# Performance work log

Hardware: AMD Instinct MI355X
Metric: run time of the kernel (lower is better)

The kernel has to match this reference:

```python
import jax, jax.numpy as jnp
import numpy as np

B, D, K = 8192, 512, 4096
MAX_WORD_LENGTH = 16
RESIDUAL_THRESHOLD = 0.01
DECAY_FACTOR = 0.95
EPS_TARGET = 1e-8


def setup_inputs() -> dict:
    key = jax.random.key(0)
    k1, k2 = jax.random.split(key)
    targets = jax.random.normal(k1, (B, D), dtype=jnp.float32)
    codebook = jax.random.normal(k2, (K, D), dtype=jnp.float32)
    return {"targets": targets, "codebook": codebook}


def reference(targets, codebook):
    """Batched greedy residual pursuit (allow_negative_signs=True).

    Returns:
      seq      [B, L] int32 signed indices (>=0: add idx; <0: subtract (-idx-1)); 0 where inactive
      mask     [B, L] bool, True where a step actually emitted a symbol
      residual [B, D] final residual after pursuit
    """
    target_norm = jnp.linalg.norm(targets, axis=-1)  # [B]

    def step(residual, step_idx):
        rnorm = jnp.linalg.norm(residual, axis=-1)  # [B]
        active = (rnorm >= RESIDUAL_THRESHOLD) & (target_norm >= EPS_TARGET)
        # cosine similarity of each codebook vector with residual direction
        res_dir = residual / jnp.maximum(rnorm, 1e-12)[:, None]
        cos = jnp.einsum('bd,kd->bk', res_dir, codebook)  # [B, K]
        best = jnp.argmax(jnp.abs(cos), axis=-1)  # [B]
        best_cos = jnp.take_along_axis(cos, best[:, None], axis=-1)[:, 0]
        signed = jnp.where(best_cos >= 0, best, -(best + 1)).astype(jnp.int32)
        sign = jnp.where(best_cos >= 0, 1.0, -1.0).astype(residual.dtype)
        decay = jnp.power(jnp.asarray(DECAY_FACTOR, residual.dtype),
                          (step_idx + 1).astype(residual.dtype))
        contrib = sign[:, None] * decay * codebook[best]  # [B, D]
        new_res = jnp.where(active[:, None], residual - contrib, residual)
        out_idx = jnp.where(active, signed, 0)
        return new_res, (out_idx, active)

    residual, (seq, mask) = jax.lax.scan(step, targets, jnp.arange(MAX_WORD_LENGTH))
    return seq.T, mask.T, residual
```

## Files before the change

kernel.cpp:

```cpp
#include <hip/hip_runtime.h>
#include <hip/hip_bf16.h>

#define B_SZ 8192
#define D_SZ 512
#define K_SZ 4096
#define L_SZ 16
#define M_ALL (B_SZ + K_SZ)

typedef __attribute__((ext_vector_type(8))) short short8v;
typedef __attribute__((ext_vector_type(4))) float f32x4;
typedef _Float16 half8v __attribute__((ext_vector_type(8)));
typedef _Float16 h2 __attribute__((ext_vector_type(2)));
struct H2x4 { h2 a, b, c, d; };

static __device__ __forceinline__ h2 habs2(h2 a) {
    unsigned u = __builtin_bit_cast(unsigned, a) & 0x7FFF7FFFu;
    return __builtin_bit_cast(h2, u);
}
static __device__ __forceinline__ h2 hmax2(h2 a, h2 b) {
#if __has_builtin(__builtin_elementwise_max)
    return __builtin_elementwise_max(a, b);
#else
    h2 r; r[0] = a[0] > b[0] ? a[0] : b[0]; r[1] = a[1] > b[1] ? a[1] : b[1]; return r;
#endif
}

__global__ void cast_bf16_kernel(const float* __restrict__ targets,
                                 const float* __restrict__ codebook,
                                 __hip_bfloat16* __restrict__ abf) {
    int idx = blockIdx.x * blockDim.x + threadIdx.x;
    const int total4 = (M_ALL * D_SZ) / 4;
    if (idx >= total4) return;
    int base = idx * 4;
    const float* src = (base < B_SZ * D_SZ) ? (targets + base)
                                            : (codebook + (base - B_SZ * D_SZ));
    float4 v = *(const float4*)src;
    abf[base + 0] = __float2bfloat16(v.x);
    abf[base + 1] = __float2bfloat16(v.y);
    abf[base + 2] = __float2bfloat16(v.z);
    abf[base + 3] = __float2bfloat16(v.w);
}

__global__ void cn2_kernel(const float* __restrict__ codebook,
                           double* __restrict__ cn2) {
    int row  = blockIdx.x * 4 + (threadIdx.x >> 6);
    int lane = threadIdx.x & 63;
    const float* r = codebook + (size_t)row * D_SZ;
    double s = 0.0;
#pragma unroll
    for (int j = 0; j < 8; j++) { double v = (double)r[lane + 64 * j]; s += v * v; }
#pragma unroll
    for (int o = 32; o > 0; o >>= 1) s += __shfl_down(s, o, 64);
    if (lane == 0) cn2[row] = s;
}

#define BM 128
#define BN 128
#define BK 32
#define LDSS 40

__global__ __launch_bounds__(256, 2)
void gemm_bt_kernel(const __hip_bfloat16* __restrict__ A,
                    const __hip_bfloat16* __restrict__ Bm,
                    _Float16* __restrict__ C) {
    __shared__ short As[BM * LDSS];
    __shared__ short Bs[BN * LDSS];
    const int tid  = threadIdx.x;
    const int bm   = blockIdx.y * BM;
    const int bn   = blockIdx.x * BN;
    const int wave = tid >> 6, lane = tid & 63;
    const int wm = (wave & 1) * 64, wn = (wave >> 1) * 64;
    const int row16 = lane & 15, quad = lane >> 4;
    const int koff = quad * 8;

    f32x4 acc[4][4] = {};

    const int srow = tid >> 1;
    const int scol = (tid & 1) * 16;
    const short* Ag = (const short*)A;
    const short* Bg = (const short*)Bm;

    for (int k0 = 0; k0 < D_SZ; k0 += BK) {
        short8v a0 = *(const short8v*)(Ag + (size_t)(bm + srow) * D_SZ + k0 + scol);
        short8v a1 = *(const short8v*)(Ag + (size_t)(bm + srow) * D_SZ + k0 + scol + 8);
        short8v b0 = *(const short8v*)(Bg + (size_t)(bn + srow) * D_SZ + k0 + scol);
        short8v b1 = *(const short8v*)(Bg + (size_t)(bn + srow) * D_SZ + k0 + scol + 8);
        __syncthreads();
        *(short8v*)(As + srow * LDSS + scol)     = a0;
        *(short8v*)(As + srow * LDSS + scol + 8) = a1;
        *(short8v*)(Bs + srow * LDSS + scol)     = b0;
        *(short8v*)(Bs + srow * LDSS + scol + 8) = b1;
        __syncthreads();

        short8v af[4], bf[4];
#pragma unroll
        for (int i = 0; i < 4; i++)
            af[i] = *(const short8v*)(As + (wm + i * 16 + row16) * LDSS + koff);
#pragma unroll
        for (int j = 0; j < 4; j++)
            bf[j] = *(const short8v*)(Bs + (wn + j * 16 + row16) * LDSS + koff);
#pragma unroll
        for (int i = 0; i < 4; i++)
#pragma unroll
            for (int j = 0; j < 4; j++)
                acc[i][j] = __builtin_amdgcn_mfma_f32_16x16x32_bf16(af[i], bf[j], acc[i][j], 0, 0, 0);
    }

#pragma unroll
    for (int i = 0; i < 4; i++) {
        int grow = bm + wm + i * 16 + quad * 4;
#pragma unroll
        for (int j = 0; j < 4; j++) {
            int gcol = bn + wn + j * 16 + row16;
#pragma unroll
            for (int r = 0; r < 4; r++)
                C[(size_t)(grow + r) * K_SZ + gcol] = (_Float16)acc[i][j][r];
        }
    }
}

#define MAXC 16
#define MARGIN 1.5f

__global__ __launch_bounds__(256, 4)
void pursuit_kernel(const float* __restrict__ targets,
                    const float* __restrict__ codebook,
                    const _Float16* __restrict__ S,
                    const double* __restrict__ cn2,
                    float* __restrict__ out) {
    const int wave = threadIdx.x >> 6;
    const int lane = threadIdx.x & 63;
    const int b = blockIdx.x * 4 + wave;
    const int lane8 = lane * 8;

    __shared__ alignas(16) _Float16 g_s[4][K_SZ];
    __shared__ int s_cnt[4];
    __shared__ int s_cand[4][MAXC];
    _Float16* g = g_s[wave];
    int* cnt  = &s_cnt[wave];
    int* cand = s_cand[wave];

    h2 tmax; tmax[0] = (_Float16)0; tmax[1] = (_Float16)0;
    {
        const _Float16* g0 = S + (size_t)b * K_SZ + lane8;
#pragma unroll
        for (int c = 0; c < 8; c++) {
            half8v h = *(const half8v*)(g0 + c * 512);
            *(half8v*)&g[c * 512 + lane8] = h;
            H2x4 u = __builtin_bit_cast(H2x4, h);
            tmax = hmax2(tmax, hmax2(hmax2(habs2(u.a), habs2(u.b)),
                                     hmax2(habs2(u.c), habs2(u.d))));
        }
    }
    float m = fmaxf((float)tmax[0], (float)tmax[1]);

    double rres[8];
    double loc = 0.0;
    {
        const float* tg = targets + (size_t)b * D_SZ + lane8;
        float4 t0 = *(const float4*)tg;
        float4 t1 = *(const float4*)(tg + 4);
        rres[0] = t0.x; rres[1] = t0.y; rres[2] = t0.z; rres[3] = t0.w;
        rres[4] = t1.x; rres[5] = t1.y; rres[6] = t1.z; rres[7] = t1.w;
#pragma unroll
        for (int e = 0; e < 8; e++) loc += rres[e] * rres[e];
    }
#pragma unroll
    for (int o = 32; o > 0; o >>= 1) loc += __shfl_xor(loc, o, 64);
    double rn2 = loc;
    const bool tgt_ok = (sqrt(loc) >= 1e-8);

    float* out_seq  = out + (size_t)b * L_SZ;
    float* out_mask = out + (size_t)B_SZ * L_SZ + (size_t)b * L_SZ;
    float* out_res  = out + (size_t)2 * B_SZ * L_SZ + (size_t)b * D_SZ;

    double decay = 1.0;

    for (int t = 0; t < L_SZ; t++) {
        decay *= 0.95;
        bool active = (sqrt(rn2) >= 0.01) && tgt_ok;
        if (!active) {
            if (lane == 0)
                for (int tt = t; tt < L_SZ; tt++) { out_seq[tt] = 0.0f; out_mask[tt] = 0.0f; }
            break;
        }

        float M = m;
#pragma unroll
        for (int o = 32; o > 0; o >>= 1) M = fmaxf(M, __shfl_xor(M, o, 64));
        float thr = M - MARGIN;

        if (lane == 0) *cnt = 0;
        if (m >= thr) {
#pragma unroll
            for (int c = 0; c < 8; c++) {
                half8v h = *(const half8v*)&g[c * 512 + lane8];
#pragma unroll
                for (int e = 0; e < 8; e++) {
                    float f = fabsf((float)h[e]);
                    if (f >= thr) {
                        int q = atomicAdd(cnt, 1);
                        if (q < MAXC) cand[q] = c * 512 + lane8 + e;
                    }
                }
            }
        }
        __threadfence_block();
        int nc = min(*cnt, MAXC);

        int bk; double bv;
        float4 c0, c1;
        if (nc == 1) {
            bk = __builtin_amdgcn_readfirstlane(cand[0]);
            const float* cr = codebook + (size_t)bk * D_SZ + lane8;
            c0 = *(const float4*)cr;
            c1 = *(const float4*)(cr + 4);
            double s = rres[0] * (double)c0.x + rres[1] * (double)c0.y
                     + rres[2] * (double)c0.z + rres[3] * (double)c0.w
                     + rres[4] * (double)c1.x + rres[5] * (double)c1.y
                     + rres[6] * (double)c1.z + rres[7] * (double)c1.w;
#pragma unroll
            for (int o = 32; o > 0; o >>= 1) s += __shfl_xor(s, o, 64);
            bv = s;
        } else {
            bk = -1; bv = 0.0;
            for (int ci = 0; ci < nc; ci++) {
                int k = __builtin_amdgcn_readfirstlane(cand[ci]);
                const float* cr = codebook + (size_t)k * D_SZ + lane8;
                float4 d0 = *(const float4*)cr;
                float4 d1 = *(const float4*)(cr + 4);
                double s = rres[0] * (double)d0.x + rres[1] * (double)d0.y
                         + rres[2] * (double)d0.z + rres[3] * (double)d0.w
                         + rres[4] * (double)d1.x + rres[5] * (double)d1.y
                         + rres[6] * (double)d1.z + rres[7] * (double)d1.w;
#pragma unroll
                for (int o = 32; o > 0; o >>= 1) s += __shfl_xor(s, o, 64);
                if (bk < 0 || fabs(s) > fabs(bv) ||
                    (fabs(s) == fabs(bv) && k < bk)) { bk = k; bv = s; }
            }
            const float* cr = codebook + (size_t)bk * D_SZ + lane8;
            c0 = *(const float4*)cr;
            c1 = *(const float4*)(cr + 4);
        }

        const _Float16* Gp = S + (size_t)(B_SZ + bk) * K_SZ + lane8;
        half8v Gh[8];
#pragma unroll
        for (int c = 0; c < 8; c++) Gh[c] = *(const half8v*)(Gp + c * 512);

        const double cn2bk = cn2[bk];
        double sd = ((bv >= 0.0) ? 1.0 : -1.0) * decay;
        rn2 = rn2 - 2.0 * sd * bv + sd * sd * cn2bk;
        if (lane == 0) {
            out_seq[t]  = (float)((bv >= 0.0) ? bk : (-bk - 1));
            out_mask[t] = 1.0f;
        }
        const float sdf = (float)sd;
        h2 sdh2; sdh2[0] = (_Float16)sdf; sdh2[1] = (_Float16)sdf;

        tmax[0] = (_Float16)0; tmax[1] = (_Float16)0;
#pragma unroll
        for (int c = 0; c < 8; c++) {
            half8v gv = *(const half8v*)&g[c * 512 + lane8];
            H2x4 ug = __builtin_bit_cast(H2x4, gv);
            H2x4 uG = __builtin_bit_cast(H2x4, Gh[c]);
            ug.a -= sdh2 * uG.a; ug.b -= sdh2 * uG.b;
            ug.c -= sdh2 * uG.c; ug.d -= sdh2 * uG.d;
            *(half8v*)&g[c * 512 + lane8] = __builtin_bit_cast(half8v, ug);
            tmax = hmax2(tmax, hmax2(hmax2(habs2(ug.a), habs2(ug.b)),
                                     hmax2(habs2(ug.c), habs2(ug.d))));
        }
        m = fmaxf((float)tmax[0], (float)tmax[1]);

        if (lane == 0) g[bk] = (_Float16)(float)(bv - sd * cn2bk);

        rres[0] -= sd * (double)c0.x; rres[1] -= sd * (double)c0.y;
        rres[2] -= sd * (double)c0.z; rres[3] -= sd * (double)c0.w;
        rres[4] -= sd * (double)c1.x; rres[5] -= sd * (double)c1.y;
        rres[6] -= sd * (double)c1.z; rres[7] -= sd * (double)c1.w;
    }

    {
        float4 r0, r1;
        r0.x = (float)rres[0]; r0.y = (float)rres[1]; r0.z = (float)rres[2]; r0.w = (float)rres[3];
        r1.x = (float)rres[4]; r1.y = (float)rres[5]; r1.z = (float)rres[6]; r1.w = (float)rres[7];
        *(float4*)(out_res + lane8) = r0;
        *(float4*)(out_res + lane8 + 4) = r1;
    }
}

extern "C" void kernel_launch(void* const* d_in, const int* in_sizes, int n_in,
                              void* d_out, int out_size, void* d_ws, size_t ws_size,
                              hipStream_t stream) {
    const float* targets  = (const float*)d_in[0];
    const float* codebook = (const float*)d_in[1];
    float* out = (float*)d_out;

    __hip_bfloat16* abf = (__hip_bfloat16*)d_ws;
    _Float16* S = (_Float16*)((char*)d_ws + (size_t)M_ALL * D_SZ * 2);
    double* cn2 = (double*)((char*)d_ws + (size_t)M_ALL * D_SZ * 2
                                        + (size_t)M_ALL * K_SZ * 2);

    int total4 = (M_ALL * D_SZ) / 4;
    cast_bf16_kernel<<<(total4 + 255) / 256, 256, 0, stream>>>(targets, codebook, abf);
    cn2_kernel<<<K_SZ / 4, 256, 0, stream>>>(codebook, cn2);

    dim3 ggrid(K_SZ / BN, M_ALL / BM);
    gemm_bt_kernel<<<ggrid, 256, 0, stream>>>(abf, abf + (size_t)B_SZ * D_SZ, S);

    pursuit_kernel<<<B_SZ / 4, 256, 0, stream>>>(targets, codebook, S, cn2, out);
}
```

Measured before the change: 343.1 us.

## Use direct global-to-LDS loads in GEMM and nontemporal hints for streaming data

The GEMM staging now uses global_load_lds, moving bf16 tiles straight into shared memory without a register round trip. The padded LDS stride is dropped and the occupancy hint removed. Output stores for the target-rows part of S, along with pursuit's one-shot loads and output stores, become nontemporal to keep the reused codebook Gram rows resident in cache. The Gram row load is also moved into each branch so it can issue earlier, next to the codebook row load. Without padding, the LDS fragment reads may now hit bank conflicts.

```diff
diff --git a/kernel.cpp b/kernel.cpp
--- a/kernel.cpp
+++ b/kernel.cpp
@@ -12,6 +12,9 @@
 typedef _Float16 half8v __attribute__((ext_vector_type(8)));
 typedef _Float16 h2 __attribute__((ext_vector_type(2)));
 struct H2x4 { h2 a, b, c, d; };
+
+typedef const __attribute__((address_space(1))) void gvoid;
+typedef __attribute__((address_space(3))) void lvoid;
 
 static __device__ __forceinline__ h2 habs2(h2 a) {
     unsigned u = __builtin_bit_cast(unsigned, a) & 0x7FFF7FFFu;
@@ -57,14 +60,13 @@
 #define BM 128
 #define BN 128
 #define BK 32
-#define LDSS 40
-
-__global__ __launch_bounds__(256, 2)
+
+__global__ __launch_bounds__(256)
 void gemm_bt_kernel(const __hip_bfloat16* __restrict__ A,
                     const __hip_bfloat16* __restrict__ Bm,
                     _Float16* __restrict__ C) {
-    __shared__ short As[BM * LDSS];
-    __shared__ short Bs[BN * LDSS];
+    __shared__ short As[BM * BK];
+    __shared__ short Bs[BN * BK];
     const int tid  = threadIdx.x;
     const int bm   = blockIdx.y * BM;
     const int bn   = blockIdx.x * BN;
@@ -75,30 +77,32 @@
 
     f32x4 acc[4][4] = {};
 
-    const int srow = tid >> 1;
-    const int scol = (tid & 1) * 16;
     const short* Ag = (const short*)A;
     const short* Bg = (const short*)Bm;
+    const int srow = lane >> 2;
+    const int scol = (lane & 3) * 8;
 
     for (int k0 = 0; k0 < D_SZ; k0 += BK) {
-        short8v a0 = *(const short8v*)(Ag + (size_t)(bm + srow) * D_SZ + k0 + scol);
-        short8v a1 = *(const short8v*)(Ag + (size_t)(bm + srow) * D_SZ + k0 + scol + 8);
-        short8v b0 = *(const short8v*)(Bg + (size_t)(bn + srow) * D_SZ + k0 + scol);
-        short8v b1 = *(const short8v*)(Bg + (size_t)(bn + srow) * D_SZ + k0 + scol + 8);
         __syncthreads();
-        *(short8v*)(As + srow * LDSS + scol)     = a0;
-        *(short8v*)(As + srow * LDSS + scol + 8) = a1;
-        *(short8v*)(Bs + srow * LDSS + scol)     = b0;
-        *(short8v*)(Bs + srow * LDSS + scol + 8) = b1;
+#pragma unroll
+        for (int c = 0; c < 2; c++) {
+            int row = (wave * 2 + c) * 16 + srow;
+            __builtin_amdgcn_global_load_lds(
+                (gvoid*)(Ag + (size_t)(bm + row) * D_SZ + k0 + scol),
+                (lvoid*)(As + row * BK + scol), 16, 0, 0);
+            __builtin_amdgcn_global_load_lds(
+                (gvoid*)(Bg + (size_t)(bn + row) * D_SZ + k0 + scol),
+                (lvoid*)(Bs + row * BK + scol), 16, 0, 0);
+        }
         __syncthreads();
 
         short8v af[4], bf[4];
 #pragma unroll
         for (int i = 0; i < 4; i++)
-            af[i] = *(const short8v*)(As + (wm + i * 16 + row16) * LDSS + koff);
+            af[i] = *(const short8v*)(As + (wm + i * 16 + row16) * BK + koff);
 #pragma unroll
         for (int j = 0; j < 4; j++)
-            bf[j] = *(const short8v*)(Bs + (wn + j * 16 + row16) * LDSS + koff);
+            bf[j] = *(const short8v*)(Bs + (wn + j * 16 + row16) * BK + koff);
 #pragma unroll
         for (int i = 0; i < 4; i++)
 #pragma unroll
@@ -106,15 +110,30 @@
                 acc[i][j] = __builtin_amdgcn_mfma_f32_16x16x32_bf16(af[i], bf[j], acc[i][j], 0, 0, 0);
     }
 
-#pragma unroll
-    for (int i = 0; i < 4; i++) {
-        int grow = bm + wm + i * 16 + quad * 4;
-#pragma unroll
-        for (int j = 0; j < 4; j++) {
-            int gcol = bn + wn + j * 16 + row16;
-#pragma unroll
-            for (int r = 0; r < 4; r++)
-                C[(size_t)(grow + r) * K_SZ + gcol] = (_Float16)acc[i][j][r];
+    if (bm < B_SZ) {
+#pragma unroll
+        for (int i = 0; i < 4; i++) {
+            int grow = bm + wm + i * 16 + quad * 4;
+#pragma unroll
+            for (int j = 0; j < 4; j++) {
+                int gcol = bn + wn + j * 16 + row16;
+#pragma unroll
+                for (int r = 0; r < 4; r++)
+                    __builtin_nontemporal_store((_Float16)acc[i][j][r],
+                                                &C[(size_t)(grow + r) * K_SZ + gcol]);
+            }
+        }
+    } else {
+#pragma unroll
+        for (int i = 0; i < 4; i++) {
+            int grow = bm + wm + i * 16 + quad * 4;
+#pragma unroll
+            for (int j = 0; j < 4; j++) {
+                int gcol = bn + wn + j * 16 + row16;
+#pragma unroll
+                for (int r = 0; r < 4; r++)
+                    C[(size_t)(grow + r) * K_SZ + gcol] = (_Float16)acc[i][j][r];
+            }
         }
     }
 }
@@ -145,7 +164,7 @@
         const _Float16* g0 = S + (size_t)b * K_SZ + lane8;
 #pragma unroll
         for (int c = 0; c < 8; c++) {
-            half8v h = *(const half8v*)(g0 + c * 512);
+            half8v h = __builtin_nontemporal_load((const half8v*)(g0 + c * 512));
             *(half8v*)&g[c * 512 + lane8] = h;
             H2x4 u = __builtin_bit_cast(H2x4, h);
             tmax = hmax2(tmax, hmax2(hmax2(habs2(u.a), habs2(u.b)),
@@ -158,10 +177,10 @@
     double loc = 0.0;
     {
         const float* tg = targets + (size_t)b * D_SZ + lane8;
-        float4 t0 = *(const float4*)tg;
-        float4 t1 = *(const float4*)(tg + 4);
-        rres[0] = t0.x; rres[1] = t0.y; rres[2] = t0.z; rres[3] = t0.w;
-        rres[4] = t1.x; rres[5] = t1.y; rres[6] = t1.z; rres[7] = t1.w;
+        f32x4 t0 = __builtin_nontemporal_load((const f32x4*)tg);
+        f32x4 t1 = __builtin_nontemporal_load((const f32x4*)(tg + 4));
+        rres[0] = t0[0]; rres[1] = t0[1]; rres[2] = t0[2]; rres[3] = t0[3];
+        rres[4] = t1[0]; rres[5] = t1[1]; rres[6] = t1[2]; rres[7] = t1[3];
 #pragma unroll
         for (int e = 0; e < 8; e++) loc += rres[e] * rres[e];
     }
@@ -181,7 +200,10 @@
         bool active = (sqrt(rn2) >= 0.01) && tgt_ok;
         if (!active) {
             if (lane == 0)
-                for (int tt = t; tt < L_SZ; tt++) { out_seq[tt] = 0.0f; out_mask[tt] = 0.0f; }
+                for (int tt = t; tt < L_SZ; tt++) {
+                    __builtin_nontemporal_store(0.0f, &out_seq[tt]);
+                    __builtin_nontemporal_store(0.0f, &out_mask[tt]);
+                }
             break;
         }
 
@@ -210,11 +232,15 @@
 
         int bk; double bv;
         float4 c0, c1;
+        half8v Gh[8];
         if (nc == 1) {
             bk = __builtin_amdgcn_readfirstlane(cand[0]);
             const float* cr = codebook + (size_t)bk * D_SZ + lane8;
+            const _Float16* Gp = S + (size_t)(B_SZ + bk) * K_SZ + lane8;
             c0 = *(const float4*)cr;
             c1 = *(const float4*)(cr + 4);
+#pragma unroll
+            for (int c = 0; c < 8; c++) Gh[c] = *(const half8v*)(Gp + c * 512);
             double s = rres[0] * (double)c0.x + rres[1] * (double)c0.y
                      + rres[2] * (double)c0.z + rres[3] * (double)c0.w
                      + rres[4] * (double)c1.x + rres[5] * (double)c1.y
@@ -239,21 +265,19 @@
                     (fabs(s) == fabs(bv) && k < bk)) { bk = k; bv = s; }
             }
             const float* cr = codebook + (size_t)bk * D_SZ + lane8;
+            const _Float16* Gp = S + (size_t)(B_SZ + bk) * K_SZ + lane8;
             c0 = *(const float4*)cr;
             c1 = *(const float4*)(cr + 4);
-        }
-
-        const _Float16* Gp = S + (size_t)(B_SZ + bk) * K_SZ + lane8;
-        half8v Gh[8];
-#pragma unroll
-        for (int c = 0; c < 8; c++) Gh[c] = *(const half8v*)(Gp + c * 512);
+#pragma unroll
+            for (int c = 0; c < 8; c++) Gh[c] = *(const half8v*)(Gp + c * 512);
+        }
 
         const double cn2bk = cn2[bk];
         double sd = ((bv >= 0.0) ? 1.0 : -1.0) * decay;
         rn2 = rn2 - 2.0 * sd * bv + sd * sd * cn2bk;
         if (lane == 0) {
-            out_seq[t]  = (float)((bv >= 0.0) ? bk : (-bk - 1));
-            out_mask[t] = 1.0f;
+            __builtin_nontemporal_store((float)((bv >= 0.0) ? bk : (-bk - 1)), &out_seq[t]);
+            __builtin_nontemporal_store(1.0f, &out_mask[t]);
         }
         const float sdf = (float)sd;
         h2 sdh2; sdh2[0] = (_Float16)sdf; sdh2[1] = (_Float16)sdf;
@@ -281,11 +305,11 @@
     }
 
     {
-        float4 r0, r1;
-        r0.x = (float)rres[0]; r0.y = (float)rres[1]; r0.z = (float)rres[2]; r0.w = (float)rres[3];
-        r1.x = (float)rres[4]; r1.y = (float)rres[5]; r1.z = (float)rres[6]; r1.w = (float)rres[7];
-        *(float4*)(out_res + lane8) = r0;
-        *(float4*)(out_res + lane8 + 4) = r1;
+        f32x4 r0, r1;
+        r0[0] = (float)rres[0]; r0[1] = (float)rres[1]; r0[2] = (float)rres[2]; r0[3] = (float)rres[3];
+        r1[0] = (float)rres[4]; r1[1] = (float)rres[5]; r1[2] = (float)rres[6]; r1[3] = (float)rres[7];
+        __builtin_nontemporal_store(r0, (f32x4*)(out_res + lane8));
+        __builtin_nontemporal_store(r1, (f32x4*)(out_res + lane8 + 4));
     }
 }
 
```

After: 335.5 us. -2.2%, faster.
